# Kernel optimization log

Hardware: AMD Instinct MI355X
Metric: run time of the kernel (lower is better)

Reference implementation:

```python
import jax, jax.numpy as jnp
import numpy as np
from jax import lax

B, T, K = 1024, 512, 32


def setup_inputs() -> dict:
    key = jax.random.key(0)
    k1, k2, k3 = jax.random.split(key, 3)
    labels = jax.random.randint(k1, (B, T), 0, K, dtype=jnp.int32)
    y_pred = jax.random.normal(k2, (B, T, K), dtype=jnp.float32)
    # glorot-uniform-ish transition matrix
    limit = np.sqrt(6.0 / (K + K)).astype(np.float32)
    trans = jax.random.uniform(k3, (K, K), minval=-limit, maxval=limit, dtype=jnp.float32)
    mask = jnp.ones((B, T), dtype=jnp.float32)
    return {"labels": labels, "y_pred": y_pred, "trans": trans, "mask": mask}


def crf_loss(labels, y_pred, trans, mask):
    n_tags = trans.shape[0]
    y_true = jax.nn.one_hot(labels, n_tags, dtype=y_pred.dtype)  # [B,T,K]
    y_true = y_true * mask[:, :, None]  # sequence_masking with value 0

    # --- target path score ---
    point_score = jnp.einsum('bni,bni->b', y_true, y_pred)
    trans_score = jnp.einsum('bni,ij,bnj->b', y_true[:, :-1], trans, y_true[:, 1:])
    target = point_score + trans_score

    # --- log partition via forward algorithm (logsumexp scan) ---
    alpha0 = y_pred[:, 0]  # [B,K]

    def step(alpha, xs):
        emit, m = xs  # emit: [B,K], m: [B,1]
        new = jax.nn.logsumexp(alpha[:, :, None] + trans[None], axis=1) + emit
        alpha = m * new + (1.0 - m) * alpha
        return alpha, None

    xs = (jnp.swapaxes(y_pred[:, 1:], 0, 1),          # [T-1,B,K]
          jnp.swapaxes(mask[:, 1:, None], 0, 1))      # [T-1,B,1]
    alpha, _ = lax.scan(step, alpha0, xs)
    log_norm = jax.nn.logsumexp(alpha, axis=1)  # [B]
    return log_norm - target


def reference(labels, y_pred, trans, mask):
    return crf_loss(labels, y_pred, trans, mask)
```

## Files before the change

### kernel.cpp

```cpp
#include <hip/hip_runtime.h>


#define K32 32
#define Tt  512
#define NCH 8
#define CHL 64

typedef float  float4v __attribute__((ext_vector_type(4)));
typedef short  short8v __attribute__((ext_vector_type(8)));

__device__ inline float bf2f_lo(unsigned d) { return __uint_as_float(d << 16); }
__device__ inline float bf2f_hi(unsigned d) { return __uint_as_float(d & 0xFFFF0000u); }

__device__ inline unsigned pack_trunc(float hi, float lo) {
    return __builtin_amdgcn_perm(__float_as_uint(hi), __float_as_uint(lo), 0x07060302u);
}
__device__ inline unsigned short f2bf_rne(float x) {
    unsigned u = __float_as_uint(x);
    return (unsigned short)((u + 0x7FFFu + ((u >> 16) & 1u)) >> 16);
}

union F8 { unsigned u[4]; short8v v; };

__global__ __launch_bounds__(256, 8) void crf_chunk(
    const int*   __restrict__ labels,
    const float* __restrict__ y_pred,
    const float* __restrict__ trans,
    const float* __restrict__ mask,
    unsigned*    __restrict__ wsMT,
    float*       __restrict__ wsS,
    float*       __restrict__ wsSc)
{
    __shared__ unsigned short NcmAll[4][32 * 40];

    const int lane = threadIdx.x & 63;
    const int wv   = threadIdx.x >> 6;
    const int gw   = blockIdx.x * 4 + wv;
    const int n    = lane & 15;
    const int q    = lane >> 4;
    const int seq  = gw >> 3;
    const int c    = gw & 7;

    unsigned short* Ncm = NcmAll[wv];

    const float* yp  = y_pred + (size_t)seq * Tt * K32;
    const int*   lb  = labels + (size_t)seq * Tt;
    const float* mkp = mask   + (size_t)seq * Tt;

    float sc;
    float mlane;
    {
        const int t = c * CHL + lane;
        const int   lab0 = lb[t];
        mlane = mkp[t];
        sc = yp[t * K32 + lab0] * mlane;
        if (t < Tt - 1) {
            sc += trans[lab0 * K32 + lb[t + 1]] * (mlane * mkp[t + 1]);
        }
#pragma unroll
        for (int s = 1; s < 64; s <<= 1) sc += __shfl_xor(sc, s, 64);
    }

    unsigned long long mbits = __ballot(mlane != 0.0f);
    if (c == 0) mbits &= ~1ull;

    F8 AE0, AE1;
#pragma unroll
    for (int h = 0; h < 4; ++h) {
        const int k0 = (h < 2) ? (q * 4 + 2 * h) : (16 + q * 4 + 2 * (h - 2));
        const int k1 = k0 + 1;
        AE0.u[h] = ((unsigned)f2bf_rne(__expf(trans[k0 * K32 + n]) * 0.03125f)) |
                   (((unsigned)f2bf_rne(__expf(trans[k1 * K32 + n]) * 0.03125f)) << 16);
        AE1.u[h] = ((unsigned)f2bf_rne(__expf(trans[k0 * K32 + 16 + n]) * 0.03125f)) |
                   (((unsigned)f2bf_rne(__expf(trans[k1 * K32 + 16 + n]) * 0.03125f)) << 16);
    }

    F8 B0, B1;
#pragma unroll
    for (int h = 0; h < 4; ++h) {
        const int r0 = (h < 2) ? (q * 4 + 2 * h) : (16 + q * 4 + 2 * (h - 2));
        const int r1 = r0 + 1;
        unsigned w0 = 0, w1 = 0;
        if (r0 == n)      w0 |= 0x3F80u;
        if (r1 == n)      w0 |= 0x3F800000u;
        if (r0 == 16 + n) w1 |= 0x3F80u;
        if (r1 == 16 + n) w1 |= 0x3F800000u;
        B0.u[h] = w0;
        B1.u[h] = w1;
    }

    float Slog    = 0.0f;
    int   applied = 0;

    const float4* ypr0 = (const float4*)(yp + q * 4);
    const float4* ypr1 = (const float4*)(yp + 16 + q * 4);

    const int tbase = c * CHL;
    const int tmax  = tbase + CHL - 1;

    float4 eA0 = ypr0[(size_t)tbase * 8],       eA1 = ypr1[(size_t)tbase * 8];
    float4 eB0 = ypr0[(size_t)(tbase + 1) * 8], eB1 = ypr1[(size_t)(tbase + 1) * 8];

    auto dostep = [&](int t, const float4& e0, const float4& e1) {
        if ((mbits >> (t & 63)) & 1ull) {
            float4v c00 = {0.f, 0.f, 0.f, 0.f}, c01 = {0.f, 0.f, 0.f, 0.f};
            float4v c10 = {0.f, 0.f, 0.f, 0.f}, c11 = {0.f, 0.f, 0.f, 0.f};
            c00 = __builtin_amdgcn_mfma_f32_16x16x32_bf16(AE0.v, B0.v, c00, 0, 0, 0);
            c01 = __builtin_amdgcn_mfma_f32_16x16x32_bf16(AE0.v, B1.v, c01, 0, 0, 0);
            c10 = __builtin_amdgcn_mfma_f32_16x16x32_bf16(AE1.v, B0.v, c10, 0, 0, 0);
            c11 = __builtin_amdgcn_mfma_f32_16x16x32_bf16(AE1.v, B1.v, c11, 0, 0, 0);

            const float4v sv0 = {__expf(e0.x), __expf(e0.y), __expf(e0.z), __expf(e0.w)};
            const float4v sv1 = {__expf(e1.x), __expf(e1.y), __expf(e1.z), __expf(e1.w)};
            c00 *= sv0; c01 *= sv0; c10 *= sv1; c11 *= sv1;

            if ((applied & 7) == 7) {
                const float cn = __uint_as_float(
                    __builtin_amdgcn_readfirstlane(__float_as_uint(c00[0])));
                const float rs = 1.0f / cn;
                c00 *= rs; c01 *= rs; c10 *= rs; c11 *= rs;
                Slog += __logf(cn);
            }
            ++applied;

            B0.u[0] = pack_trunc(c00[1], c00[0]);
            B0.u[1] = pack_trunc(c00[3], c00[2]);
            B0.u[2] = pack_trunc(c10[1], c10[0]);
            B0.u[3] = pack_trunc(c10[3], c10[2]);
            B1.u[0] = pack_trunc(c01[1], c01[0]);
            B1.u[1] = pack_trunc(c01[3], c01[2]);
            B1.u[2] = pack_trunc(c11[1], c11[0]);
            B1.u[3] = pack_trunc(c11[3], c11[2]);
        }
    };

    for (int i = 0; i < CHL; i += 2) {
        const int t = tbase + i;
        dostep(t, eA0, eA1);
        {
            const int tn = (t + 2 <= tmax) ? (t + 2) : tmax;
            eA0 = ypr0[(size_t)tn * 8]; eA1 = ypr1[(size_t)tn * 8];
        }
        dostep(t + 1, eB0, eB1);
        {
            const int tn = (t + 3 <= tmax) ? (t + 3) : tmax;
            eB0 = ypr0[(size_t)tn * 8]; eB1 = ypr1[(size_t)tn * 8];
        }
    }

    {
        unsigned* Nd = (unsigned*)Ncm;
        *(uint2*)&Nd[n * 20 + q * 2]            = make_uint2(B0.u[0], B0.u[1]);
        *(uint2*)&Nd[n * 20 + 8 + q * 2]        = make_uint2(B0.u[2], B0.u[3]);
        *(uint2*)&Nd[(16 + n) * 20 + q * 2]     = make_uint2(B1.u[0], B1.u[1]);
        *(uint2*)&Nd[(16 + n) * 20 + 8 + q * 2] = make_uint2(B1.u[2], B1.u[3]);
    }
    unsigned* md = wsMT + (size_t)gw * 512;
    for (int idx = lane; idx < 512; idx += 64) {
        const int k = idx >> 4, d = idx & 15;
        const unsigned lo = Ncm[(2 * d) * 40 + k];
        const unsigned hi = Ncm[(2 * d + 1) * 40 + k];
        md[idx] = lo | (hi << 16);
    }
    if (lane == 0) {
        wsS[gw]  = Slog + (float)applied * 3.46573590f;
        wsSc[gw] = sc;
    }
}

__global__ __launch_bounds__(64) void crf_combine(
    const float*    __restrict__ y_pred,
    const unsigned* __restrict__ wsMT,
    const float*    __restrict__ wsS,
    const float*    __restrict__ wsSc,
    float*          __restrict__ out)
{
    const int lane = threadIdx.x;
    const int h    = lane >> 5;
    const int j    = lane & 31;
    const int seq  = blockIdx.x;

    const uint4* mb = (const uint4*)(wsMT + (size_t)seq * NCH * 512);
    uint4 mA[NCH], mB[NCH];
#pragma unroll
    for (int cc = 0; cc < NCH; ++cc) {
        mA[cc] = mb[cc * 128 + j * 4 + 2 * h];
        mB[cc] = mb[cc * 128 + j * 4 + 2 * h + 1];
    }

    const float* yp = y_pred + (size_t)seq * Tt * K32;
    const float a0 = yp[j];
    const float m0 = __shfl(a0, 0, 64);
    float p = __expf(a0 - m0);
    float S = m0;

    float scs = 0.0f;
#pragma unroll
    for (int cc = 0; cc < NCH; ++cc) {
        S   += wsS[seq * NCH + cc];
        scs += wsSc[seq * NCH + cc];
    }

    const int cb = h << 4;
#pragma unroll
    for (int cc = 0; cc < NCH; ++cc) {
        const float cn = __shfl(p, 0, 64);
        const unsigned u0 = mA[cc].x, u1 = mA[cc].y, u2 = mA[cc].z, u3 = mA[cc].w;
        const unsigned u4 = mB[cc].x, u5 = mB[cc].y, u6 = mB[cc].z, u7 = mB[cc].w;
        float acc = 0.0f;
        acc = fmaf(__shfl(p, cb +  0, 64), bf2f_lo(u0), acc);
        acc = fmaf(__shfl(p, cb +  1, 64), bf2f_hi(u0), acc);
        acc = fmaf(__shfl(p, cb +  2, 64), bf2f_lo(u1), acc);
        acc = fmaf(__shfl(p, cb +  3, 64), bf2f_hi(u1), acc);
        acc = fmaf(__shfl(p, cb +  4, 64), bf2f_lo(u2), acc);
        acc = fmaf(__shfl(p, cb +  5, 64), bf2f_hi(u2), acc);
        acc = fmaf(__shfl(p, cb +  6, 64), bf2f_lo(u3), acc);
        acc = fmaf(__shfl(p, cb +  7, 64), bf2f_hi(u3), acc);
        acc = fmaf(__shfl(p, cb +  8, 64), bf2f_lo(u4), acc);
        acc = fmaf(__shfl(p, cb +  9, 64), bf2f_hi(u4), acc);
        acc = fmaf(__shfl(p, cb + 10, 64), bf2f_lo(u5), acc);
        acc = fmaf(__shfl(p, cb + 11, 64), bf2f_hi(u5), acc);
        acc = fmaf(__shfl(p, cb + 12, 64), bf2f_lo(u6), acc);
        acc = fmaf(__shfl(p, cb + 13, 64), bf2f_hi(u6), acc);
        acc = fmaf(__shfl(p, cb + 14, 64), bf2f_lo(u7), acc);
        acc = fmaf(__shfl(p, cb + 15, 64), bf2f_hi(u7), acc);
        acc += __shfl_xor(acc, 32, 64);
        p = acc * (1.0f / cn);
        S += __logf(cn);
    }

    float sp = p;
    sp += __shfl_xor(sp,  1, 64);
    sp += __shfl_xor(sp,  2, 64);
    sp += __shfl_xor(sp,  4, 64);
    sp += __shfl_xor(sp,  8, 64);
    sp += __shfl_xor(sp, 16, 64);

    if (lane == 0) {
        out[seq] = S + __logf(sp) - scs;
    }
}

extern "C" void kernel_launch(void* const* d_in, const int* in_sizes, int n_in,
                              void* d_out, int out_size, void* d_ws, size_t ws_size,
                              hipStream_t stream) {
    const int*   labels = (const int*)  d_in[0];
    const float* y_pred = (const float*)d_in[1];
    const float* trans  = (const float*)d_in[2];
    const float* mask   = (const float*)d_in[3];
    float* out = (float*)d_out;

    unsigned* wsMT = (unsigned*)d_ws;
    float* wsS  = (float*)((char*)d_ws + (size_t)1024 * NCH * 512 * 4);
    float* wsSc = wsS + 1024 * NCH;

    crf_chunk<<<2048, 256, 0, stream>>>(labels, y_pred, trans, mask, wsMT, wsS, wsSc);
    crf_combine<<<1024, 64, 0, stream>>>(y_pred, wsMT, wsS, wsSc, out);
}
```

Baseline: 165.3 us.

## Load one emission per lane, share exp via bpermute, deepen prefetch to 8 steps

Each lane now loads a single scalar emission (lane&31) per time step instead of two float4s. It computes one exp and distributes the values to the MFMA row layout with ds_bpermute. The prefetch depth grows from 2 to 8 time steps, and the wave index is made uniform with readfirstlane. The aim is to cut redundant exp work and per-step load latency on the serial recurrence, at the cost of 8 LDS-permute operations per step on the critical path.

```diff
diff --git a/kernel.cpp b/kernel.cpp
--- a/kernel.cpp
+++ b/kernel.cpp
@@ -18,6 +18,10 @@
 __device__ inline unsigned short f2bf_rne(float x) {
     unsigned u = __float_as_uint(x);
     return (unsigned short)((u + 0x7FFFu + ((u >> 16) & 1u)) >> 16);
+}
+
+__device__ inline float bperm(int idx, float v) {
+    return __int_as_float(__builtin_amdgcn_ds_bpermute(idx, __float_as_int(v)));
 }
 
 union F8 { unsigned u[4]; short8v v; };
@@ -34,7 +38,7 @@
     __shared__ unsigned short NcmAll[4][32 * 40];
 
     const int lane = threadIdx.x & 63;
-    const int wv   = threadIdx.x >> 6;
+    const int wv   = __builtin_amdgcn_readfirstlane(threadIdx.x >> 6);
     const int gw   = blockIdx.x * 4 + wv;
     const int n    = lane & 15;
     const int q    = lane >> 4;
@@ -89,19 +93,25 @@
         B1.u[h] = w1;
     }
 
+    const int ix0 = (q * 4 + 0) << 2;
+    const int ix1 = (q * 4 + 1) << 2;
+    const int ix2 = (q * 4 + 2) << 2;
+    const int ix3 = (q * 4 + 3) << 2;
+    const int jx0 = ix0 + 64, jx1 = ix1 + 64, jx2 = ix2 + 64, jx3 = ix3 + 64;
+
     float Slog    = 0.0f;
     int   applied = 0;
 
-    const float4* ypr0 = (const float4*)(yp + q * 4);
-    const float4* ypr1 = (const float4*)(yp + 16 + q * 4);
-
     const int tbase = c * CHL;
     const int tmax  = tbase + CHL - 1;
-
-    float4 eA0 = ypr0[(size_t)tbase * 8],       eA1 = ypr1[(size_t)tbase * 8];
-    float4 eB0 = ypr0[(size_t)(tbase + 1) * 8], eB1 = ypr1[(size_t)(tbase + 1) * 8];
-
-    auto dostep = [&](int t, const float4& e0, const float4& e1) {
+    const int ln32  = lane & 31;
+
+    auto L = [&](int t) -> float { return yp[t * K32 + ln32]; };
+
+    float ev0 = L(tbase + 0), ev1 = L(tbase + 1), ev2 = L(tbase + 2), ev3 = L(tbase + 3);
+    float ev4 = L(tbase + 4), ev5 = L(tbase + 5), ev6 = L(tbase + 6), ev7 = L(tbase + 7);
+
+    auto dostep = [&](int t, float ev) {
         if ((mbits >> (t & 63)) & 1ull) {
             float4v c00 = {0.f, 0.f, 0.f, 0.f}, c01 = {0.f, 0.f, 0.f, 0.f};
             float4v c10 = {0.f, 0.f, 0.f, 0.f}, c11 = {0.f, 0.f, 0.f, 0.f};
@@ -110,8 +120,9 @@
             c10 = __builtin_amdgcn_mfma_f32_16x16x32_bf16(AE1.v, B0.v, c10, 0, 0, 0);
             c11 = __builtin_amdgcn_mfma_f32_16x16x32_bf16(AE1.v, B1.v, c11, 0, 0, 0);
 
-            const float4v sv0 = {__expf(e0.x), __expf(e0.y), __expf(e0.z), __expf(e0.w)};
-            const float4v sv1 = {__expf(e1.x), __expf(e1.y), __expf(e1.z), __expf(e1.w)};
+            const float pe = __expf(ev);
+            const float4v sv0 = {bperm(ix0, pe), bperm(ix1, pe), bperm(ix2, pe), bperm(ix3, pe)};
+            const float4v sv1 = {bperm(jx0, pe), bperm(jx1, pe), bperm(jx2, pe), bperm(jx3, pe)};
             c00 *= sv0; c01 *= sv0; c10 *= sv1; c11 *= sv1;
 
             if ((applied & 7) == 7) {
@@ -134,18 +145,16 @@
         }
     };
 
-    for (int i = 0; i < CHL; i += 2) {
+    for (int i = 0; i < CHL; i += 8) {
         const int t = tbase + i;
-        dostep(t, eA0, eA1);
-        {
-            const int tn = (t + 2 <= tmax) ? (t + 2) : tmax;
-            eA0 = ypr0[(size_t)tn * 8]; eA1 = ypr1[(size_t)tn * 8];
-        }
-        dostep(t + 1, eB0, eB1);
-        {
-            const int tn = (t + 3 <= tmax) ? (t + 3) : tmax;
-            eB0 = ypr0[(size_t)tn * 8]; eB1 = ypr1[(size_t)tn * 8];
-        }
+        dostep(t + 0, ev0);  ev0 = L(min(t +  8, tmax));
+        dostep(t + 1, ev1);  ev1 = L(min(t +  9, tmax));
+        dostep(t + 2, ev2);  ev2 = L(min(t + 10, tmax));
+        dostep(t + 3, ev3);  ev3 = L(min(t + 11, tmax));
+        dostep(t + 4, ev4);  ev4 = L(min(t + 12, tmax));
+        dostep(t + 5, ev5);  ev5 = L(min(t + 13, tmax));
+        dostep(t + 6, ev6);  ev6 = L(min(t + 14, tmax));
+        dostep(t + 7, ev7);  ev7 = L(min(t + 15, tmax));
     }
 
     {
```

Result: faster. 153.6 us (-7.1%).

## Stage exp of emissions in LDS with coalesced prefetch, halve chunk count

Applied to the files above, without the earlier changes.

Each wave now processes a 128-step chunk (4 chunks per sequence instead of 8), loading 64 timesteps of emissions with coalesced float4 loads into registers, exponentiating them in bulk into LDS, and prefetching the next segment. The serial MFMA recurrence then reads the precomputed exp values from LDS instead of issuing per-step strided global loads and exps. A fully-masked fast path drops the per-step mask test. The combine kernel does fewer chunk merges, but half as many waves run, each with a longer serial chain and more LDS per block, which lowers occupancy.

```diff
diff --git a/kernel.cpp b/kernel.cpp
--- a/kernel.cpp
+++ b/kernel.cpp
@@ -3,8 +3,9 @@
 
 #define K32 32
 #define Tt  512
-#define NCH 8
-#define CHL 64
+#define NCH 4
+#define CHL 128
+#define NSEG 2
 
 typedef float  float4v __attribute__((ext_vector_type(4)));
 typedef short  short8v __attribute__((ext_vector_type(8)));
@@ -22,7 +23,7 @@
 
 union F8 { unsigned u[4]; short8v v; };
 
-__global__ __launch_bounds__(256, 8) void crf_chunk(
+__global__ __launch_bounds__(256, 4) void crf_chunk(
     const int*   __restrict__ labels,
     const float* __restrict__ y_pred,
     const float* __restrict__ trans,
@@ -31,38 +32,47 @@
     float*       __restrict__ wsS,
     float*       __restrict__ wsSc)
 {
-    __shared__ unsigned short NcmAll[4][32 * 40];
+    __shared__ float expAll[4][64 * 32];
 
     const int lane = threadIdx.x & 63;
-    const int wv   = threadIdx.x >> 6;
+    const int wv   = __builtin_amdgcn_readfirstlane(threadIdx.x >> 6);
     const int gw   = blockIdx.x * 4 + wv;
     const int n    = lane & 15;
     const int q    = lane >> 4;
-    const int seq  = gw >> 3;
-    const int c    = gw & 7;
-
-    unsigned short* Ncm = NcmAll[wv];
+    const int seq  = gw >> 2;
+    const int c    = gw & 3;
+
+    float* eb = &expAll[wv][0];
 
     const float* yp  = y_pred + (size_t)seq * Tt * K32;
     const int*   lb  = labels + (size_t)seq * Tt;
     const float* mkp = mask   + (size_t)seq * Tt;
-
-    float sc;
-    float mlane;
+    const int tbase = c * CHL;
+
+    float4 pre[8];
     {
-        const int t = c * CHL + lane;
-        const int   lab0 = lb[t];
-        mlane = mkp[t];
-        sc = yp[t * K32 + lab0] * mlane;
+        const float4* gs = (const float4*)(yp + (size_t)tbase * K32);
+#pragma unroll
+        for (int jj = 0; jj < 8; ++jj) pre[jj] = gs[jj * 64 + lane];
+    }
+
+    unsigned long long mb[NSEG];
+    float sc = 0.0f;
+#pragma unroll
+    for (int s = 0; s < NSEG; ++s) {
+        const int t = tbase + s * 64 + lane;
+        const int lab0 = lb[t];
+        const float mlane = mkp[t];
+        float scl = yp[t * K32 + lab0] * mlane;
         if (t < Tt - 1) {
-            sc += trans[lab0 * K32 + lb[t + 1]] * (mlane * mkp[t + 1]);
-        }
-#pragma unroll
-        for (int s = 1; s < 64; s <<= 1) sc += __shfl_xor(sc, s, 64);
-    }
-
-    unsigned long long mbits = __ballot(mlane != 0.0f);
-    if (c == 0) mbits &= ~1ull;
+            scl += trans[lab0 * K32 + lb[t + 1]] * (mlane * mkp[t + 1]);
+        }
+        sc += scl;
+        mb[s] = __ballot(mlane != 0.0f);
+    }
+    if (c == 0) mb[0] &= ~1ull;
+#pragma unroll
+    for (int s = 1; s < 64; s <<= 1) sc += __shfl_xor(sc, s, 64);
 
     F8 AE0, AE1;
 #pragma unroll
@@ -92,69 +102,75 @@
     float Slog    = 0.0f;
     int   applied = 0;
 
-    const float4* ypr0 = (const float4*)(yp + q * 4);
-    const float4* ypr1 = (const float4*)(yp + 16 + q * 4);
-
-    const int tbase = c * CHL;
-    const int tmax  = tbase + CHL - 1;
-
-    float4 eA0 = ypr0[(size_t)tbase * 8],       eA1 = ypr1[(size_t)tbase * 8];
-    float4 eB0 = ypr0[(size_t)(tbase + 1) * 8], eB1 = ypr1[(size_t)(tbase + 1) * 8];
-
-    auto dostep = [&](int t, const float4& e0, const float4& e1) {
-        if ((mbits >> (t & 63)) & 1ull) {
-            float4v c00 = {0.f, 0.f, 0.f, 0.f}, c01 = {0.f, 0.f, 0.f, 0.f};
-            float4v c10 = {0.f, 0.f, 0.f, 0.f}, c11 = {0.f, 0.f, 0.f, 0.f};
-            c00 = __builtin_amdgcn_mfma_f32_16x16x32_bf16(AE0.v, B0.v, c00, 0, 0, 0);
-            c01 = __builtin_amdgcn_mfma_f32_16x16x32_bf16(AE0.v, B1.v, c01, 0, 0, 0);
-            c10 = __builtin_amdgcn_mfma_f32_16x16x32_bf16(AE1.v, B0.v, c10, 0, 0, 0);
-            c11 = __builtin_amdgcn_mfma_f32_16x16x32_bf16(AE1.v, B1.v, c11, 0, 0, 0);
-
-            const float4v sv0 = {__expf(e0.x), __expf(e0.y), __expf(e0.z), __expf(e0.w)};
-            const float4v sv1 = {__expf(e1.x), __expf(e1.y), __expf(e1.z), __expf(e1.w)};
-            c00 *= sv0; c01 *= sv0; c10 *= sv1; c11 *= sv1;
-
-            if ((applied & 7) == 7) {
-                const float cn = __uint_as_float(
-                    __builtin_amdgcn_readfirstlane(__float_as_uint(c00[0])));
-                const float rs = 1.0f / cn;
-                c00 *= rs; c01 *= rs; c10 *= rs; c11 *= rs;
-                Slog += __logf(cn);
+    const int svoff0 = q * 4;
+    const int svoff1 = 16 + q * 4;
+
+    auto body = [&](int i) {
+        const float4v sv0 = *(const float4v*)&eb[i * 32 + svoff0];
+        const float4v sv1 = *(const float4v*)&eb[i * 32 + svoff1];
+
+        float4v c00 = {0.f, 0.f, 0.f, 0.f}, c01 = {0.f, 0.f, 0.f, 0.f};
+        float4v c10 = {0.f, 0.f, 0.f, 0.f}, c11 = {0.f, 0.f, 0.f, 0.f};
+        c00 = __builtin_amdgcn_mfma_f32_16x16x32_bf16(AE0.v, B0.v, c00, 0, 0, 0);
+        c01 = __builtin_amdgcn_mfma_f32_16x16x32_bf16(AE0.v, B1.v, c01, 0, 0, 0);
+        c10 = __builtin_amdgcn_mfma_f32_16x16x32_bf16(AE1.v, B0.v, c10, 0, 0, 0);
+        c11 = __builtin_amdgcn_mfma_f32_16x16x32_bf16(AE1.v, B1.v, c11, 0, 0, 0);
+
+        c00 *= sv0; c01 *= sv0; c10 *= sv1; c11 *= sv1;
+
+        if ((applied & 7) == 7) {
+            const float cn = __uint_as_float(
+                __builtin_amdgcn_readfirstlane(__float_as_uint(c00[0])));
+            const float rs = 1.0f / cn;
+            c00 *= rs; c01 *= rs; c10 *= rs; c11 *= rs;
+            Slog += __logf(cn);
+        }
+        ++applied;
+
+        B0.u[0] = pack_trunc(c00[1], c00[0]);
+        B0.u[1] = pack_trunc(c00[3], c00[2]);
+        B0.u[2] = pack_trunc(c10[1], c10[0]);
+        B0.u[3] = pack_trunc(c10[3], c10[2]);
+        B1.u[0] = pack_trunc(c01[1], c01[0]);
+        B1.u[1] = pack_trunc(c01[3], c01[2]);
+        B1.u[2] = pack_trunc(c11[1], c11[0]);
+        B1.u[3] = pack_trunc(c11[3], c11[2]);
+    };
+
+    for (int seg = 0; seg < NSEG; ++seg) {
+#pragma unroll
+        for (int jj = 0; jj < 8; ++jj) {
+            float4v e;
+            e[0] = __expf(pre[jj].x); e[1] = __expf(pre[jj].y);
+            e[2] = __expf(pre[jj].z); e[3] = __expf(pre[jj].w);
+            *(float4v*)&eb[(jj * 64 + lane) * 4] = e;
+        }
+        if (seg + 1 < NSEG) {
+            const float4* gs = (const float4*)(yp + (size_t)(tbase + (seg + 1) * 64) * K32);
+#pragma unroll
+            for (int jj = 0; jj < 8; ++jj) pre[jj] = gs[jj * 64 + lane];
+        }
+
+        const unsigned long long mbits = mb[seg];
+        if (mbits == ~0ull) {
+#pragma unroll 8
+            for (int i = 0; i < 64; ++i) body(i);
+        } else {
+#pragma unroll 4
+            for (int i = 0; i < 64; ++i) {
+                if ((mbits >> i) & 1ull) body(i);
             }
-            ++applied;
-
-            B0.u[0] = pack_trunc(c00[1], c00[0]);
-            B0.u[1] = pack_trunc(c00[3], c00[2]);
-            B0.u[2] = pack_trunc(c10[1], c10[0]);
-            B0.u[3] = pack_trunc(c10[3], c10[2]);
-            B1.u[0] = pack_trunc(c01[1], c01[0]);
-            B1.u[1] = pack_trunc(c01[3], c01[2]);
-            B1.u[2] = pack_trunc(c11[1], c11[0]);
-            B1.u[3] = pack_trunc(c11[3], c11[2]);
-        }
-    };
-
-    for (int i = 0; i < CHL; i += 2) {
-        const int t = tbase + i;
-        dostep(t, eA0, eA1);
-        {
-            const int tn = (t + 2 <= tmax) ? (t + 2) : tmax;
-            eA0 = ypr0[(size_t)tn * 8]; eA1 = ypr1[(size_t)tn * 8];
-        }
-        dostep(t + 1, eB0, eB1);
-        {
-            const int tn = (t + 3 <= tmax) ? (t + 3) : tmax;
-            eB0 = ypr0[(size_t)tn * 8]; eB1 = ypr1[(size_t)tn * 8];
         }
     }
 
     {
-        unsigned* Nd = (unsigned*)Ncm;
+        unsigned* Nd = (unsigned*)eb;
         *(uint2*)&Nd[n * 20 + q * 2]            = make_uint2(B0.u[0], B0.u[1]);
         *(uint2*)&Nd[n * 20 + 8 + q * 2]        = make_uint2(B0.u[2], B0.u[3]);
         *(uint2*)&Nd[(16 + n) * 20 + q * 2]     = make_uint2(B1.u[0], B1.u[1]);
         *(uint2*)&Nd[(16 + n) * 20 + 8 + q * 2] = make_uint2(B1.u[2], B1.u[3]);
     }
+    const unsigned short* Ncm = (const unsigned short*)eb;
     unsigned* md = wsMT + (size_t)gw * 512;
     for (int idx = lane; idx < 512; idx += 64) {
         const int k = idx >> 4, d = idx & 15;
@@ -254,6 +270,6 @@
     float* wsS  = (float*)((char*)d_ws + (size_t)1024 * NCH * 512 * 4);
     float* wsSc = wsS + 1024 * NCH;
 
-    crf_chunk<<<2048, 256, 0, stream>>>(labels, y_pred, trans, mask, wsMT, wsS, wsSc);
+    crf_chunk<<<1024, 256, 0, stream>>>(labels, y_pred, trans, mask, wsMT, wsS, wsSc);
     crf_combine<<<1024, 64, 0, stream>>>(y_pred, wsMT, wsS, wsSc, out);
 }
```

New measurement: 143.0 us. 13.5% less time.
